# Kernel optimization log

Hardware: AMD Instinct MI355X
Metric: run time of the kernel (lower is better)

Reference implementation:

```python
import jax, jax.numpy as jnp
import numpy as np
from jax import lax

NPOINT, RADIUS, NSAMPLE, K_KEY = 64, 1.0, 32, 64

def conv1d(x, W, b):
    # 1x1 Conv1d: x [B,Cin,N], W [Cout,Cin], b [Cout] -> [B,Cout,N]
    return jnp.einsum('bcn,dc->bdn', x, W) + b[None, :, None]

def farthest_point_sample(xyz, npoint):
    # xyz [B,N,3] -> idx [B,npoint]
    B, N, _ = xyz.shape
    dist0 = jnp.full((B, N), 1e10, dtype=xyz.dtype)
    far0 = jnp.zeros((B,), dtype=jnp.int32)
    def body(carry, _):
        dist, far = carry
        centroid = jnp.take_along_axis(xyz, far[:, None, None].astype(jnp.int32), axis=1)  # [B,1,3]
        d = jnp.sum((xyz - centroid) ** 2, -1)
        dist = jnp.minimum(dist, d)
        nxt = jnp.argmax(dist, -1).astype(jnp.int32)
        return (dist, nxt), far
    _, idxs = lax.scan(body, (dist0, far0), None, length=npoint)
    return idxs.T  # [B,npoint]

def ball_query(radius, nsample, xyz, new_xyz):
    # xyz [B,N,3], new_xyz [B,S,3] -> group_idx [B,S,nsample]
    N = xyz.shape[1]
    sqr = jnp.sum((new_xyz[:, :, None, :] - xyz[:, None, :, :]) ** 2, -1)  # [B,S,N]
    gidx = jnp.where(sqr > radius ** 2, N, jnp.arange(N, dtype=jnp.int32)[None, None, :])
    gidx = jnp.sort(gidx, axis=-1)[..., :nsample]
    first = gidx[..., :1]
    gidx = jnp.where(gidx == N, first, gidx)
    return gidx

def sample_and_group(npoint, radius, nsample, xyz, points):
    # xyz [B,N,3], points [B,N,D]
    B = xyz.shape[0]
    fps_idx = farthest_point_sample(xyz, npoint)                     # [B,S]
    bidx = jnp.arange(B)[:, None]
    new_xyz = xyz[bidx, fps_idx]                                     # [B,S,3]
    gidx = ball_query(radius, nsample, xyz, new_xyz)                 # [B,S,ns]
    bidx2 = jnp.arange(B)[:, None, None]
    grouped_xyz = xyz[bidx2, gidx]                                   # [B,S,ns,3]
    grouped_xyz_norm = grouped_xyz - new_xyz[:, :, None, :]
    grouped_points = points[bidx2, gidx]                             # [B,S,ns,D]
    new_points = jnp.concatenate([grouped_xyz_norm, grouped_points], axis=-1)
    return new_xyz, new_points

def setup_inputs() -> dict:
    key = jax.random.key(0)
    ks = jax.random.split(key, 12)
    B, C, N = 8, 6, 65536
    def w(k, co, ci):
        return jax.random.normal(k, (co, ci), jnp.float32) * (1.0 / np.sqrt(ci))
    return {
        'src_pts': jax.random.normal(ks[0], (B, C, N), jnp.float32),
        'tgt_pts': jax.random.normal(ks[1], (B, C, N), jnp.float32),
        'W1': w(ks[2], 32, 6),  'b1': jnp.zeros((32,), jnp.float32),
        'W2': w(ks[3], 64, 32), 'b2': jnp.zeros((64,), jnp.float32),
        'Wa': w(ks[4], 16, 64), 'ba': jnp.zeros((16,), jnp.float32),
        'Wb': w(ks[5], 8, 16),  'bb': jnp.zeros((8,), jnp.float32),
        'Wc': w(ks[6], 1, 8),   'bc': jnp.zeros((1,), jnp.float32),
    }

def reference(src_pts, tgt_pts, W1, b1, W2, b2, Wa, ba, Wb, bb, Wc, bc):
    # feat_extraction_layer: 1x1 conv stack over points -> deep per-point features
    h = jax.nn.relu(conv1d(src_pts, W1, b1))            # [B,32,N]
    deep_feat_pts = jax.nn.relu(conv1d(h, W2, b2))      # [B,64,N]
    # weighting_layer: per-point saliency weight + top-k keypoint indices (1-D, batch-0 idiom)
    w = jax.nn.relu(conv1d(deep_feat_pts, Wa, ba))
    w = jax.nn.relu(conv1d(w, Wb, bb))
    w = jax.nn.softplus(conv1d(w, Wc, bc))              # [B,1,N]
    _, keypts_idx = lax.top_k(w[0, 0], K_KEY)           # [K]
    # irregular keypoint gather (shared index across batch, as in src_pts[:, :, idx])
    src_keypts = src_pts[:, :, keypts_idx].transpose(0, 2, 1)   # [B,K,C]
    # ball-query sample_and_group on keypoints (computed then discarded, as in original)
    _gxyz, _gpts = sample_and_group(NPOINT, RADIUS, NSAMPLE, src_keypts[:, :, :3], src_keypts[:, :, 3:])
    return src_keypts
```

## Files before the change

kernel.cpp:

```cpp
#include <hip/hip_runtime.h>
#include <stdint.h>

#define N_PTS 65536
#define NB1 32768
#define NB2 4096
#define CAND_CAP 4096
#define FCAP 1024
typedef unsigned long long u64;


__global__ __launch_bounds__(256) void zero_kernel(uint4* __restrict__ z, int n4)
{
    const int i = blockIdx.x * 256 + threadIdx.x;
    const uint4 zz = {0u, 0u, 0u, 0u};
    if (i < n4) z[i] = zz;
}

__global__ __launch_bounds__(256, 1) void score_kernel(
    const float* __restrict__ src,
    const float* __restrict__ W1, const float* __restrict__ b1,
    const float* __restrict__ W2, const float* __restrict__ b2,
    const float* __restrict__ Wa, const float* __restrict__ ba,
    const float* __restrict__ Wb, const float* __restrict__ bb,
    const float* __restrict__ Wc, const float* __restrict__ bc,
    float* __restrict__ scores, unsigned* __restrict__ hist1)
{
    __shared__ unsigned histL[NB1];
    __shared__ __align__(16) float sW1[32 * 8];
    __shared__ __align__(16) float sW2[64 * 32];
    __shared__ __align__(16) float sWaT[64 * 16];
    __shared__ __align__(16) float sWb[8 * 16];
    __shared__ float sb2[64], sba[16], sbb[8], sWc[8], sbc1[1];
    const int t = threadIdx.x;

    {
        uint4* h4 = (uint4*)histL;
        const uint4 zz = {0u, 0u, 0u, 0u};
        #pragma unroll
        for (int i = 0; i < 32; i++) h4[t + 256 * i] = zz;
    }
    {
        const int j = t >> 3, c = t & 7;
        sW1[t] = (c < 6) ? W1[j * 6 + c] : ((c == 6) ? b1[j] : 0.f);
    }
    for (int i = t; i < 2048; i += 256) sW2[i] = W2[i];
    for (int i = t; i < 1024; i += 256) {
        const int j = i >> 4, q = i & 15;
        sWaT[i] = Wa[q * 64 + j];
    }
    if (t < 128) sWb[t] = Wb[t];
    if (t < 64)  sb2[t] = b2[t];
    if (t < 16)  sba[t] = ba[t];
    if (t < 8)   { sbb[t] = bb[t]; sWc[t] = Wc[t]; }
    if (t == 0)  sbc1[0] = bc[0];
    __syncthreads();

    const int base = blockIdx.x * 512;
    const int p[2] = { base + t, base + 256 + t };

    float x[2][6];
    #pragma unroll
    for (int c = 0; c < 6; c++) {
        x[0][c] = src[c * N_PTS + p[0]];
        x[1][c] = src[c * N_PTS + p[1]];
    }

    float h1[2][32];
    #pragma unroll
    for (int j = 0; j < 32; j++) {
        const float4 wA = *(const float4*)&sW1[j * 8];
        const float4 wB = *(const float4*)&sW1[j * 8 + 4];
        #pragma unroll
        for (int P = 0; P < 2; P++) {
            float a = wB.z;
            a = fmaf(wA.x, x[P][0], a); a = fmaf(wA.y, x[P][1], a);
            a = fmaf(wA.z, x[P][2], a); a = fmaf(wA.w, x[P][3], a);
            a = fmaf(wB.x, x[P][4], a); a = fmaf(wB.y, x[P][5], a);
            h1[P][j] = fmaxf(a, 0.f);
        }
    }

    float h3[2][16];
    #pragma unroll
    for (int q = 0; q < 16; q++) { h3[0][q] = sba[q]; h3[1][q] = sba[q]; }

    #pragma unroll 1
    for (int jb = 0; jb < 32; jb++) {
        const int j0 = 2 * jb, j1 = j0 + 1;
        const float4* r0 = (const float4*)&sW2[j0 * 32];
        const float4* r1 = (const float4*)&sW2[j1 * 32];
        const float4* wa0 = (const float4*)&sWaT[j0 * 16];
        const float4* wa1 = (const float4*)&sWaT[j1 * 16];
        float4 u[8], v[8], q0[4], q1[4];
        #pragma unroll
        for (int i = 0; i < 8; i++) u[i] = r0[i];
        #pragma unroll
        for (int i = 0; i < 8; i++) v[i] = r1[i];
        #pragma unroll
        for (int i = 0; i < 4; i++) q0[i] = wa0[i];
        #pragma unroll
        for (int i = 0; i < 4; i++) q1[i] = wa1[i];
        const float bj0 = sb2[j0], bj1 = sb2[j1];

        #pragma unroll
        for (int P = 0; P < 2; P++) {
            float a0 = 0.f, a1 = 0.f, a2 = 0.f, a3 = 0.f;
            float c0 = 0.f, c1 = 0.f, c2 = 0.f, c3 = 0.f;
            #pragma unroll
            for (int i4 = 0; i4 < 8; i4++) {
                const float h0 = h1[P][4 * i4 + 0], hh1 = h1[P][4 * i4 + 1];
                const float h2 = h1[P][4 * i4 + 2], hh3 = h1[P][4 * i4 + 3];
                a0 = fmaf(u[i4].x, h0, a0); a1 = fmaf(u[i4].y, hh1, a1);
                a2 = fmaf(u[i4].z, h2, a2); a3 = fmaf(u[i4].w, hh3, a3);
                c0 = fmaf(v[i4].x, h0, c0); c1 = fmaf(v[i4].y, hh1, c1);
                c2 = fmaf(v[i4].z, h2, c2); c3 = fmaf(v[i4].w, hh3, c3);
            }
            const float v0 = fmaxf((a0 + a1) + (a2 + a3) + bj0, 0.f);
            const float v1 = fmaxf((c0 + c1) + (c2 + c3) + bj1, 0.f);
            #pragma unroll
            for (int q4 = 0; q4 < 4; q4++) {
                float t0 = h3[P][4 * q4 + 0], t1 = h3[P][4 * q4 + 1];
                float t2 = h3[P][4 * q4 + 2], t3 = h3[P][4 * q4 + 3];
                t0 = fmaf(q0[q4].x, v0, t0); t1 = fmaf(q0[q4].y, v0, t1);
                t2 = fmaf(q0[q4].z, v0, t2); t3 = fmaf(q0[q4].w, v0, t3);
                t0 = fmaf(q1[q4].x, v1, t0); t1 = fmaf(q1[q4].y, v1, t1);
                t2 = fmaf(q1[q4].z, v1, t2); t3 = fmaf(q1[q4].w, v1, t3);
                h3[P][4 * q4 + 0] = t0; h3[P][4 * q4 + 1] = t1;
                h3[P][4 * q4 + 2] = t2; h3[P][4 * q4 + 3] = t3;
            }
        }
    }
    #pragma unroll
    for (int q = 0; q < 16; q++) {
        h3[0][q] = fmaxf(h3[0][q], 0.f);
        h3[1][q] = fmaxf(h3[1][q], 0.f);
    }

    float z[2] = { sbc1[0], sbc1[0] };
    #pragma unroll
    for (int j = 0; j < 8; j++) {
        const float4* wbr = (const float4*)&sWb[j * 16];
        const float4 w0 = wbr[0], w1 = wbr[1], w2 = wbr[2], w3 = wbr[3];
        const float bj = sbb[j], wc = sWc[j];
        #pragma unroll
        for (int P = 0; P < 2; P++) {
            float s0 = bj, s1 = 0.f, s2 = 0.f, s3 = 0.f;
            s0 = fmaf(w0.x, h3[P][0],  s0); s1 = fmaf(w0.y, h3[P][1],  s1);
            s2 = fmaf(w0.z, h3[P][2],  s2); s3 = fmaf(w0.w, h3[P][3],  s3);
            s0 = fmaf(w1.x, h3[P][4],  s0); s1 = fmaf(w1.y, h3[P][5],  s1);
            s2 = fmaf(w1.z, h3[P][6],  s2); s3 = fmaf(w1.w, h3[P][7],  s3);
            s0 = fmaf(w2.x, h3[P][8],  s0); s1 = fmaf(w2.y, h3[P][9],  s1);
            s2 = fmaf(w2.z, h3[P][10], s2); s3 = fmaf(w2.w, h3[P][11], s3);
            s0 = fmaf(w3.x, h3[P][12], s0); s1 = fmaf(w3.y, h3[P][13], s1);
            s2 = fmaf(w3.z, h3[P][14], s2); s3 = fmaf(w3.w, h3[P][15], s3);
            z[P] = fmaf(wc, fmaxf((s0 + s1) + (s2 + s3), 0.f), z[P]);
        }
    }

    #pragma unroll
    for (int P = 0; P < 2; P++) {
        const float sp = fmaxf(z[P], 0.f) + log1pf(expf(-fabsf(z[P])));
        scores[p[P]] = sp;
        atomicAdd(&histL[__float_as_uint(sp) >> 16], 1u);
    }
    __syncthreads();

    for (int i = t; i < NB1; i += 256) {
        const unsigned v = histL[i];
        if (v) atomicAdd(&hist1[i], v);
    }
}

__global__ __launch_bounds__(256) void refine_kernel(
    const unsigned* __restrict__ hist1, const float* __restrict__ scores,
    unsigned* __restrict__ hist2, int* __restrict__ meta,
    u64* __restrict__ cand)
{
    __shared__ unsigned csum[256];
    __shared__ unsigned bsum[128];
    __shared__ int sh_c, sh_B;
    __shared__ unsigned sh_tail;
    const int t = threadIdx.x;

    {
        unsigned s = 0;
        const uint4* h4 = (const uint4*)(hist1 + t * 128);
        #pragma unroll
        for (int i = 0; i < 32; i++) {
            const uint4 v = h4[i];
            s += v.x + v.y + v.z + v.w;
        }
        csum[t] = s;
    }
    __syncthreads();
    for (int d = 1; d < 256; d <<= 1) {
        const unsigned v = (t + d < 256) ? csum[t + d] : 0u;
        __syncthreads();
        csum[t] += v;
        __syncthreads();
    }
    {
        const unsigned here = csum[t];
        const unsigned nxt = (t + 1 < 256) ? csum[t + 1] : 0u;
        if (here >= 64u && nxt < 64u) sh_c = t;
    }
    __syncthreads();
    const int cstar = sh_c;
    if (t < 128) bsum[t] = hist1[cstar * 128 + t];
    __syncthreads();
    {
        const unsigned ctail = (cstar + 1 < 256) ? csum[cstar + 1] : 0u;
        for (int d = 1; d < 128; d <<= 1) {
            unsigned v = 0u;
            if (t < 128 && t + d < 128) v = bsum[t + d];
            __syncthreads();
            if (t < 128) bsum[t] += v;
            __syncthreads();
        }
        if (t < 128) {
            const unsigned here = bsum[t] + ctail;
            const unsigned nxt = (t + 1 < 128) ? bsum[t + 1] + ctail : ctail;
            if (here >= 64u && nxt < 64u) { sh_B = cstar * 128 + t; sh_tail = nxt; }
        }
    }
    __syncthreads();
    const unsigned Bstar = (unsigned)sh_B;
    if (blockIdx.x == 0 && t == 0) { meta[0] = sh_B; meta[1] = (int)sh_tail; }

    const float4* s4 = (const float4*)scores;
    const int i = blockIdx.x * 256 + t;
    const float4 v = s4[i];
    const int n0 = 4 * i;
    #pragma unroll
    for (int k = 0; k < 4; k++) {
        const float sv = (k == 0) ? v.x : (k == 1) ? v.y : (k == 2) ? v.z : v.w;
        const unsigned b = __float_as_uint(sv);
        const unsigned hi = b >> 16;
        if (hi >= Bstar) {
            const int p = atomicAdd(&meta[2], 1);
            if (p < CAND_CAP) cand[p] = ((u64)b << 32) | (unsigned)~(n0 + k);
            if (hi == Bstar) atomicAdd(&hist2[(b & 0xFFFFu) >> 4], 1u);
        }
    }
}

__global__ __launch_bounds__(256) void final_kernel(
    const unsigned* __restrict__ hist2, const int* __restrict__ meta,
    const u64* __restrict__ cand, const float* __restrict__ src,
    float* __restrict__ out)
{
    __shared__ unsigned h2[NB2];
    __shared__ unsigned csum[256];
    __shared__ u64 keys[FCAP];
    __shared__ int idxs[64];
    __shared__ int sh_c, sh_T2, sh_cnt;
    const int t = threadIdx.x;
    const unsigned Bstar = (unsigned)meta[0];
    const unsigned tail1 = (unsigned)meta[1];

    {
        uint4* d = (uint4*)h2;
        const uint4* s = (const uint4*)hist2;
        #pragma unroll
        for (int i = 0; i < 4; i++) d[t + 256 * i] = s[t + 256 * i];
    }
    __syncthreads();

    {
        unsigned s = 0;
        #pragma unroll
        for (int i = 0; i < 16; i++) s += h2[t * 16 + i];
        csum[t] = s;
    }
    __syncthreads();
    for (int d = 1; d < 256; d <<= 1) {
        const unsigned v = (t + d < 256) ? csum[t + d] : 0u;
        __syncthreads();
        csum[t] += v;
        __syncthreads();
    }
    {
        const unsigned here = tail1 + csum[t];
        const unsigned nxt = tail1 + ((t + 1 < 256) ? csum[t + 1] : 0u);
        if (here >= 64u && nxt < 64u) sh_c = t;
    }
    __syncthreads();
    {
        const int c2 = sh_c;
        if (t == 0) {
            unsigned acc = tail1 + ((c2 + 1 < 256) ? csum[c2 + 1] : 0u);
            int T2 = c2 * 16;
            for (int b = c2 * 16 + 15; b >= c2 * 16; b--) {
                acc += h2[b];
                if (acc >= 64u) { T2 = b; break; }
            }
            sh_T2 = T2;
            sh_cnt = 0;
        }
    }
    __syncthreads();
    const unsigned T2 = (unsigned)sh_T2;

    int count = meta[2];
    if (count > CAND_CAP) count = CAND_CAP;
    for (int i = t; i < count; i += 256) {
        const u64 key = cand[i];
        const unsigned b = (unsigned)(key >> 32);
        const unsigned hi = b >> 16;
        if (hi > Bstar || ((b & 0xFFFFu) >> 4) >= T2) {
            const int p = atomicAdd(&sh_cnt, 1);
            if (p < FCAP) keys[p] = key;
        }
    }
    __syncthreads();

    int fcnt = sh_cnt;
    if (fcnt > FCAP) fcnt = FCAP;
    for (int i = t; i < fcnt; i += 256) {
        const u64 me = keys[i];
        int r = 0;
        for (int j = 0; j < fcnt; j++) r += (keys[j] > me);
        if (r < 64) idxs[r] = (int)~(unsigned)(me & 0xFFFFFFFFu);
    }
    __syncthreads();

    for (int e = t; e < 3072; e += 256) {
        const int b  = e / 384;
        const int rr = e % 384;
        const int kk = rr / 6;
        const int c  = rr % 6;
        out[e] = src[(b * 6 + c) * N_PTS + idxs[kk]];
    }
}

extern "C" void kernel_launch(void* const* d_in, const int* in_sizes, int n_in,
                              void* d_out, int out_size, void* d_ws, size_t ws_size,
                              hipStream_t stream)
{
    const float* src = (const float*)d_in[0];
    const float* W1 = (const float*)d_in[2];
    const float* b1 = (const float*)d_in[3];
    const float* W2 = (const float*)d_in[4];
    const float* b2 = (const float*)d_in[5];
    const float* Wa = (const float*)d_in[6];
    const float* ba = (const float*)d_in[7];
    const float* Wb = (const float*)d_in[8];
    const float* bb = (const float*)d_in[9];
    const float* Wc = (const float*)d_in[10];
    const float* bc = (const float*)d_in[11];

    char* ws = (char*)d_ws;
    float*    scores = (float*)ws;
    unsigned* hist1  = (unsigned*)(ws + 256 * 1024);
    unsigned* hist2  = (unsigned*)(ws + 384 * 1024);
    int*      meta   = (int*)(ws + 400 * 1024);
    u64*      cand   = (u64*)(ws + 408 * 1024);
    float*    out    = (float*)d_out;

    const int n4 = (NB1 + NB2 + 16) / 4;
    zero_kernel<<<(n4 + 255) / 256, 256, 0, stream>>>((uint4*)hist1, n4);
    score_kernel<<<128, 256, 0, stream>>>(src, W1, b1, W2, b2, Wa, ba,
                                          Wb, bb, Wc, bc, scores, hist1);
    refine_kernel<<<64, 256, 0, stream>>>(hist1, scores, hist2, meta, cand);
    final_kernel<<<1, 256, 0, stream>>>(hist2, meta, cand, src, out);
}
```

Before: 135.6 us.

## Pack block-local histogram into 16-bit counters and process one point per thread

The score kernel now handles one point per thread across twice as many blocks (256 instead of 128). The shared-memory histogram is packed as two 16-bit counters per word, halving its LDS footprint so two blocks can be resident per CU, and launch bounds are raised to allow that. The goal is more blocks to cover the 256 CUs and better latency hiding. In exchange there is less per-thread instruction-level parallelism, each point still needs its own weight loads from shared memory, and twice as many blocks each flush their histogram with global atomics.

```diff
diff --git a/kernel.cpp b/kernel.cpp
--- a/kernel.cpp
+++ b/kernel.cpp
@@ -16,7 +16,7 @@
     if (i < n4) z[i] = zz;
 }
 
-__global__ __launch_bounds__(256, 1) void score_kernel(
+__global__ __launch_bounds__(256, 2) void score_kernel(
     const float* __restrict__ src,
     const float* __restrict__ W1, const float* __restrict__ b1,
     const float* __restrict__ W2, const float* __restrict__ b2,
@@ -25,7 +25,7 @@
     const float* __restrict__ Wc, const float* __restrict__ bc,
     float* __restrict__ scores, unsigned* __restrict__ hist1)
 {
-    __shared__ unsigned histL[NB1];
+    __shared__ unsigned histL[NB1 / 2];
     __shared__ __align__(16) float sW1[32 * 8];
     __shared__ __align__(16) float sW2[64 * 32];
     __shared__ __align__(16) float sWaT[64 * 16];
@@ -37,7 +37,7 @@
         uint4* h4 = (uint4*)histL;
         const uint4 zz = {0u, 0u, 0u, 0u};
         #pragma unroll
-        for (int i = 0; i < 32; i++) h4[t + 256 * i] = zz;
+        for (int i = 0; i < 16; i++) h4[t + 256 * i] = zz;
     }
     {
         const int j = t >> 3, c = t & 7;
@@ -55,34 +55,27 @@
     if (t == 0)  sbc1[0] = bc[0];
     __syncthreads();
 
-    const int base = blockIdx.x * 512;
-    const int p[2] = { base + t, base + 256 + t };
-
-    float x[2][6];
-    #pragma unroll
-    for (int c = 0; c < 6; c++) {
-        x[0][c] = src[c * N_PTS + p[0]];
-        x[1][c] = src[c * N_PTS + p[1]];
-    }
-
-    float h1[2][32];
+    const int p = blockIdx.x * 256 + t;
+
+    float x[6];
+    #pragma unroll
+    for (int c = 0; c < 6; c++) x[c] = src[c * N_PTS + p];
+
+    float h1[32];
     #pragma unroll
     for (int j = 0; j < 32; j++) {
         const float4 wA = *(const float4*)&sW1[j * 8];
         const float4 wB = *(const float4*)&sW1[j * 8 + 4];
-        #pragma unroll
-        for (int P = 0; P < 2; P++) {
-            float a = wB.z;
-            a = fmaf(wA.x, x[P][0], a); a = fmaf(wA.y, x[P][1], a);
-            a = fmaf(wA.z, x[P][2], a); a = fmaf(wA.w, x[P][3], a);
-            a = fmaf(wB.x, x[P][4], a); a = fmaf(wB.y, x[P][5], a);
-            h1[P][j] = fmaxf(a, 0.f);
-        }
-    }
-
-    float h3[2][16];
-    #pragma unroll
-    for (int q = 0; q < 16; q++) { h3[0][q] = sba[q]; h3[1][q] = sba[q]; }
+        float a = wB.z;
+        a = fmaf(wA.x, x[0], a); a = fmaf(wA.y, x[1], a);
+        a = fmaf(wA.z, x[2], a); a = fmaf(wA.w, x[3], a);
+        a = fmaf(wB.x, x[4], a); a = fmaf(wB.y, x[5], a);
+        h1[j] = fmaxf(a, 0.f);
+    }
+
+    float h3[16];
+    #pragma unroll
+    for (int q = 0; q < 16; q++) h3[q] = sba[q];
 
     #pragma unroll 1
     for (int jb = 0; jb < 32; jb++) {
@@ -102,72 +95,74 @@
         for (int i = 0; i < 4; i++) q1[i] = wa1[i];
         const float bj0 = sb2[j0], bj1 = sb2[j1];
 
-        #pragma unroll
-        for (int P = 0; P < 2; P++) {
-            float a0 = 0.f, a1 = 0.f, a2 = 0.f, a3 = 0.f;
-            float c0 = 0.f, c1 = 0.f, c2 = 0.f, c3 = 0.f;
-            #pragma unroll
-            for (int i4 = 0; i4 < 8; i4++) {
-                const float h0 = h1[P][4 * i4 + 0], hh1 = h1[P][4 * i4 + 1];
-                const float h2 = h1[P][4 * i4 + 2], hh3 = h1[P][4 * i4 + 3];
-                a0 = fmaf(u[i4].x, h0, a0); a1 = fmaf(u[i4].y, hh1, a1);
-                a2 = fmaf(u[i4].z, h2, a2); a3 = fmaf(u[i4].w, hh3, a3);
-                c0 = fmaf(v[i4].x, h0, c0); c1 = fmaf(v[i4].y, hh1, c1);
-                c2 = fmaf(v[i4].z, h2, c2); c3 = fmaf(v[i4].w, hh3, c3);
-            }
-            const float v0 = fmaxf((a0 + a1) + (a2 + a3) + bj0, 0.f);
-            const float v1 = fmaxf((c0 + c1) + (c2 + c3) + bj1, 0.f);
-            #pragma unroll
-            for (int q4 = 0; q4 < 4; q4++) {
-                float t0 = h3[P][4 * q4 + 0], t1 = h3[P][4 * q4 + 1];
-                float t2 = h3[P][4 * q4 + 2], t3 = h3[P][4 * q4 + 3];
-                t0 = fmaf(q0[q4].x, v0, t0); t1 = fmaf(q0[q4].y, v0, t1);
-                t2 = fmaf(q0[q4].z, v0, t2); t3 = fmaf(q0[q4].w, v0, t3);
-                t0 = fmaf(q1[q4].x, v1, t0); t1 = fmaf(q1[q4].y, v1, t1);
-                t2 = fmaf(q1[q4].z, v1, t2); t3 = fmaf(q1[q4].w, v1, t3);
-                h3[P][4 * q4 + 0] = t0; h3[P][4 * q4 + 1] = t1;
-                h3[P][4 * q4 + 2] = t2; h3[P][4 * q4 + 3] = t3;
-            }
-        }
-    }
-    #pragma unroll
-    for (int q = 0; q < 16; q++) {
-        h3[0][q] = fmaxf(h3[0][q], 0.f);
-        h3[1][q] = fmaxf(h3[1][q], 0.f);
-    }
-
-    float z[2] = { sbc1[0], sbc1[0] };
+        float a0 = 0.f, a1 = 0.f, a2 = 0.f, a3 = 0.f;
+        float c0 = 0.f, c1 = 0.f, c2 = 0.f, c3 = 0.f;
+        #pragma unroll
+        for (int i4 = 0; i4 < 8; i4++) {
+            const float h0 = h1[4 * i4 + 0], hh1 = h1[4 * i4 + 1];
+            const float h2 = h1[4 * i4 + 2], hh3 = h1[4 * i4 + 3];
+            a0 = fmaf(u[i4].x, h0, a0); a1 = fmaf(u[i4].y, hh1, a1);
+            a2 = fmaf(u[i4].z, h2, a2); a3 = fmaf(u[i4].w, hh3, a3);
+            c0 = fmaf(v[i4].x, h0, c0); c1 = fmaf(v[i4].y, hh1, c1);
+            c2 = fmaf(v[i4].z, h2, c2); c3 = fmaf(v[i4].w, hh3, c3);
+        }
+        const float v0 = fmaxf((a0 + a1) + (a2 + a3) + bj0, 0.f);
+        const float v1 = fmaxf((c0 + c1) + (c2 + c3) + bj1, 0.f);
+        #pragma unroll
+        for (int q4 = 0; q4 < 4; q4++) {
+            float t0 = h3[4 * q4 + 0], t1 = h3[4 * q4 + 1];
+            float t2 = h3[4 * q4 + 2], t3 = h3[4 * q4 + 3];
+            t0 = fmaf(q0[q4].x, v0, t0); t1 = fmaf(q0[q4].y, v0, t1);
+            t2 = fmaf(q0[q4].z, v0, t2); t3 = fmaf(q0[q4].w, v0, t3);
+            t0 = fmaf(q1[q4].x, v1, t0); t1 = fmaf(q1[q4].y, v1, t1);
+            t2 = fmaf(q1[q4].z, v1, t2); t3 = fmaf(q1[q4].w, v1, t3);
+            h3[4 * q4 + 0] = t0; h3[4 * q4 + 1] = t1;
+            h3[4 * q4 + 2] = t2; h3[4 * q4 + 3] = t3;
+        }
+    }
+    #pragma unroll
+    for (int q = 0; q < 16; q++) h3[q] = fmaxf(h3[q], 0.f);
+
+    float z = sbc1[0];
     #pragma unroll
     for (int j = 0; j < 8; j++) {
         const float4* wbr = (const float4*)&sWb[j * 16];
         const float4 w0 = wbr[0], w1 = wbr[1], w2 = wbr[2], w3 = wbr[3];
         const float bj = sbb[j], wc = sWc[j];
-        #pragma unroll
-        for (int P = 0; P < 2; P++) {
-            float s0 = bj, s1 = 0.f, s2 = 0.f, s3 = 0.f;
-            s0 = fmaf(w0.x, h3[P][0],  s0); s1 = fmaf(w0.y, h3[P][1],  s1);
-            s2 = fmaf(w0.z, h3[P][2],  s2); s3 = fmaf(w0.w, h3[P][3],  s3);
-            s0 = fmaf(w1.x, h3[P][4],  s0); s1 = fmaf(w1.y, h3[P][5],  s1);
-            s2 = fmaf(w1.z, h3[P][6],  s2); s3 = fmaf(w1.w, h3[P][7],  s3);
-            s0 = fmaf(w2.x, h3[P][8],  s0); s1 = fmaf(w2.y, h3[P][9],  s1);
-            s2 = fmaf(w2.z, h3[P][10], s2); s3 = fmaf(w2.w, h3[P][11], s3);
-            s0 = fmaf(w3.x, h3[P][12], s0); s1 = fmaf(w3.y, h3[P][13], s1);
-            s2 = fmaf(w3.z, h3[P][14], s2); s3 = fmaf(w3.w, h3[P][15], s3);
-            z[P] = fmaf(wc, fmaxf((s0 + s1) + (s2 + s3), 0.f), z[P]);
-        }
-    }
-
-    #pragma unroll
-    for (int P = 0; P < 2; P++) {
-        const float sp = fmaxf(z[P], 0.f) + log1pf(expf(-fabsf(z[P])));
-        scores[p[P]] = sp;
-        atomicAdd(&histL[__float_as_uint(sp) >> 16], 1u);
-    }
-    __syncthreads();
-
-    for (int i = t; i < NB1; i += 256) {
-        const unsigned v = histL[i];
-        if (v) atomicAdd(&hist1[i], v);
+        float s0 = bj, s1 = 0.f, s2 = 0.f, s3 = 0.f;
+        s0 = fmaf(w0.x, h3[0],  s0); s1 = fmaf(w0.y, h3[1],  s1);
+        s2 = fmaf(w0.z, h3[2],  s2); s3 = fmaf(w0.w, h3[3],  s3);
+        s0 = fmaf(w1.x, h3[4],  s0); s1 = fmaf(w1.y, h3[5],  s1);
+        s2 = fmaf(w1.z, h3[6],  s2); s3 = fmaf(w1.w, h3[7],  s3);
+        s0 = fmaf(w2.x, h3[8],  s0); s1 = fmaf(w2.y, h3[9],  s1);
+        s2 = fmaf(w2.z, h3[10], s2); s3 = fmaf(w2.w, h3[11], s3);
+        s0 = fmaf(w3.x, h3[12], s0); s1 = fmaf(w3.y, h3[13], s1);
+        s2 = fmaf(w3.z, h3[14], s2); s3 = fmaf(w3.w, h3[15], s3);
+        z = fmaf(wc, fmaxf((s0 + s1) + (s2 + s3), 0.f), z);
+    }
+
+    {
+        const float sp = fmaxf(z, 0.f) + log1pf(expf(-fabsf(z)));
+        scores[p] = sp;
+        const unsigned bin = __float_as_uint(sp) >> 16;
+        atomicAdd(&histL[bin >> 1], 1u << (16 * (bin & 1)));
+    }
+    __syncthreads();
+
+    {
+        const uint4* h4 = (const uint4*)histL;
+        for (int i = t; i < NB1 / 8; i += 256) {
+            const uint4 v = h4[i];
+            const int b0 = 8 * i;
+            const unsigned w[4] = { v.x, v.y, v.z, v.w };
+            #pragma unroll
+            for (int k = 0; k < 4; k++) {
+                const unsigned lo = w[k] & 0xFFFFu;
+                const unsigned hi = w[k] >> 16;
+                if (lo) atomicAdd(&hist1[b0 + 2 * k + 0], lo);
+                if (hi) atomicAdd(&hist1[b0 + 2 * k + 1], hi);
+            }
+        }
     }
 }
 
@@ -359,7 +354,7 @@
 
     const int n4 = (NB1 + NB2 + 16) / 4;
     zero_kernel<<<(n4 + 255) / 256, 256, 0, stream>>>((uint4*)hist1, n4);
-    score_kernel<<<128, 256, 0, stream>>>(src, W1, b1, W2, b2, Wa, ba,
+    score_kernel<<<256, 256, 0, stream>>>(src, W1, b1, W2, b2, Wa, ba,
                                           Wb, bb, Wc, bc, scores, hist1);
     refine_kernel<<<64, 256, 0, stream>>>(hist1, scores, hist2, meta, cand);
     final_kernel<<<1, 256, 0, stream>>>(hist2, meta, cand, src, out);
```

Result: slower. 157.1 us (+15.9%).
